# Kernel optimization log

Hardware: AMD Instinct MI355X
Metric: run time of the kernel (lower is better)

Reference implementation:

```python
import jax, jax.numpy as jnp
import numpy as np

CELL = 0.5          # grid_map cell size (meters)
NUM_POSES = 256     # config.num_pose_samples


def setup_inputs() -> dict:
    key = jax.random.key(0)
    k1, k2, k3, k4 = jax.random.split(key, 4)
    B, N, I, J, D = 2, 1024, 128, 128, 32
    f_q = jax.random.normal(k1, (B, N, D), jnp.float32)
    f_map = jax.random.normal(k2, (B, I, J, D), jnp.float32)
    # query frustum points: 32x32 grid, x in [-15.5, 15.5], y in [0.5, 31.5]
    xs = jnp.arange(32, dtype=jnp.float32) - 15.5
    ys = jnp.arange(32, dtype=jnp.float32) + 0.5
    grid = jnp.stack(jnp.meshgrid(xs, ys, indexing='ij'), -1).reshape(-1, 2)
    q_xy = jnp.broadcast_to(grid, (B, N, 2)).astype(jnp.float32)
    valid_q = jax.random.bernoulli(k3, 0.9, (B, N))
    valid_map = jax.random.bernoulli(k4, 0.8, (B, I, J))
    temperature = jnp.array(0.5, jnp.float32)
    return {"f_q": f_q, "f_map": f_map, "q_xy": q_xy, "temperature": temperature,
            "valid_q": valid_q, "valid_map": valid_map, "seed": 0}


def reference(f_q, f_map, q_xy, temperature, valid_q, valid_map, seed):
    B, N, D = f_q.shape
    _, I, J, _ = f_map.shape
    K = NUM_POSES

    # dense cross-correlation: [B, N, I, J]
    sim = jnp.einsum('bnd,bijd->bnij', f_q, f_map)
    sim = jax.nn.relu(sim)                      # clip_negative_scores
    sim = sim.astype(jnp.float32) * jnp.exp(temperature)
    # joint softmax over the two spatial axes
    m = sim.max(axis=(-2, -1), keepdims=True)
    e = jnp.exp(sim - m)
    prob = e / e.sum(axis=(-2, -1), keepdims=True)
    num_valid = valid_q.sum(-1).clip(min=1).astype(jnp.float32)[:, None, None, None]
    sim = sim / num_valid
    prob = prob / num_valid

    # --- RANSAC 2-point pose sampling (no gradient through prob) ---
    p = jax.lax.stop_gradient(prob)
    kq, km = jax.random.split(jax.random.key(seed))
    n_idx = jax.random.randint(kq, (B, 2 * K), 0, N)          # 2 query pts per pose
    b_idx = jnp.arange(B)[:, None]
    p_flat = p.reshape(B, N, I * J)
    rows = p_flat[b_idx, n_idx]                               # [B, 2K, IJ]
    m_flat = jax.random.categorical(km, jnp.log(rows + 1e-20), axis=-1)  # [B, 2K]
    mi, mj = m_flat // J, m_flat % J
    m_xy = (jnp.stack([mi, mj], -1).astype(jnp.float32) + 0.5) * CELL    # cell centers
    m_xy = m_xy.reshape(B, K, 2, 2)
    q_pts = q_xy[b_idx, n_idx].reshape(B, K, 2, 2)
    dq = q_pts[:, :, 1] - q_pts[:, :, 0]
    dm = m_xy[:, :, 1] - m_xy[:, :, 0]
    theta = jnp.arctan2(dm[..., 1], dm[..., 0]) - jnp.arctan2(dq[..., 1], dq[..., 0])
    c, s = jnp.cos(theta), jnp.sin(theta)
    R = jnp.stack([jnp.stack([c, -s], -1), jnp.stack([s, c], -1)], -2)   # [B,K,2,2]
    t = m_xy[:, :, 0] - jnp.einsum('bkxy,bky->bkx', R, q_pts[:, :, 0])   # [B,K,2]

    # --- score every pose hypothesis ---
    p_map = jnp.einsum('bkxy,bny->bknx', R, q_xy) + t[:, :, None]        # [B,K,N,2]
    ij = jnp.floor(p_map / CELL).astype(jnp.int32)
    inb = (ij[..., 0] >= 0) & (ij[..., 0] < I) & (ij[..., 1] >= 0) & (ij[..., 1] < J)
    flat = jnp.clip(ij[..., 0], 0, I - 1) * J + jnp.clip(ij[..., 1], 0, J - 1)  # [B,K,N]
    vmap_flat = valid_map.reshape(B, I * J)
    vgather = vmap_flat[b_idx, flat.reshape(B, K * N)].reshape(B, K, N)
    sim_flat = sim.reshape(B, N, I * J)
    sgather = jnp.take_along_axis(sim_flat, flat.transpose(0, 2, 1), axis=2)  # [B,N,K]
    mask = valid_q[:, None, :] & inb & vgather                                # [B,K,N]
    scores = jnp.sum(sgather.transpose(0, 2, 1) * mask, axis=-1)              # [B,K]
    return scores
```

## Files before the change

kernel.cpp:

```cpp
#include <hip/hip_runtime.h>
#include <stdint.h>

typedef unsigned int u32;
typedef unsigned long long u64;
typedef _Float16 f16x8 __attribute__((ext_vector_type(8)));
typedef float f32x4 __attribute__((ext_vector_type(4)));

#define IJ 16384
#define NQ 1024
#define NB 2
#define KP 256
#define NSEG 16
#define SEGW 1024
#define NT 1024

__device__ __forceinline__ void tf2x32(u32 k0, u32 k1, u32& x0, u32& x1) {
  u32 kx = k0 ^ k1 ^ 0x1BD11BDAu;
#define TFR(r) { x0 += x1; x1 = (x1 << (r)) | (x1 >> (32 - (r))); x1 ^= x0; }
  x0 += k0; x1 += k1;
  TFR(13) TFR(15) TFR(26) TFR(6)
  x0 += k1; x1 += kx + 1u;
  TFR(17) TFR(29) TFR(16) TFR(24)
  x0 += kx; x1 += k0 + 2u;
  TFR(13) TFR(15) TFR(26) TFR(6)
  x0 += k0; x1 += k1 + 3u;
  TFR(17) TFR(29) TFR(16) TFR(24)
  x0 += k1; x1 += kx + 4u;
  TFR(13) TFR(15) TFR(26) TFR(6)
  x0 += kx; x1 += k0 + 5u;
#undef TFR
}

__device__ __forceinline__ void tf_subkey(u32 k0, u32 k1, u32 i, u32& s0, u32& s1) {
  u32 x0 = 0u, x1 = i;
  tf2x32(k0, k1, x0, x1);
  s0 = x0; s1 = x1;
}

__device__ __forceinline__ u32 tf_xorbits(u32 k0, u32 k1, u32 i) {
  u32 x0 = 0u, x1 = i;
  tf2x32(k0, k1, x0, x1);
  return x0 ^ x1;
}

__device__ __forceinline__ void derive_keys(int seed, u32& kq0, u32& kq1,
                                            u32& km0, u32& km1) {
  u32 k0 = 0u;
  u32 k1 = (u32)seed;
  tf_subkey(k0, k1, 0u, kq0, kq1);
  tf_subkey(k0, k1, 1u, km0, km1);
}

__device__ __forceinline__ int derive_n(int seed, u32 s) {
  u32 kq0, kq1, km0, km1;
  derive_keys(seed, kq0, kq1, km0, km1);
  u32 l0, l1;
  tf_subkey(kq0, kq1, 1u, l0, l1);
  return (int)(tf_xorbits(l0, l1, s) & 1023u);
}

__device__ __forceinline__ float gumbel_from_bits(u32 w) {
  const float tiny = 1.17549435e-38f;
  float fl = __uint_as_float((w >> 9) | 0x3f800000u) - 1.0f;
  float u = fl * (1.0f - tiny) + tiny;
  u = fmaxf(tiny, u);
  return -logf(-logf(u));
}

__device__ __forceinline__ bool read_bool(const void* p, int idx, int is32) {
  return is32 ? (((const int*)p)[idx] != 0)
              : (((const unsigned char*)p)[idx] != 0);
}

__device__ __forceinline__ u32 fkey(float x) {
  u32 b = __float_as_uint(x);
  return b ^ ((b & 0x80000000u) ? 0xFFFFFFFFu : 0x80000000u);
}

__device__ __forceinline__ void load_split(const float* __restrict__ src,
                                           f16x8& h1, f16x8& h2) {
  float4 a = *(const float4*)src;
  float4 b = *(const float4*)(src + 16);
  float x[8] = {a.x, a.y, a.z, a.w, b.x, b.y, b.z, b.w};
#pragma unroll
  for (int e = 0; e < 8; ++e) {
    _Float16 hi = (_Float16)x[e];
    h1[e] = hi;
    h2[e] = (_Float16)((x[e] - (float)hi) * 2048.0f);
  }
}

__device__ __forceinline__ f32x4 emul_mfma(f16x8 m1, f16x8 m2, f16x8 q1,
                                           f16x8 q2) {
  const f32x4 zero4 = {0.f, 0.f, 0.f, 0.f};
  const float c11 = 4.8828125e-4f;
  f32x4 x = __builtin_amdgcn_mfma_f32_16x16x32_f16(m2, q2, zero4, 0, 0, 0);
  x *= c11;
  x = __builtin_amdgcn_mfma_f32_16x16x32_f16(m2, q1, x, 0, 0, 0);
  x = __builtin_amdgcn_mfma_f32_16x16x32_f16(m1, q2, x, 0, 0, 0);
  x *= c11;
  return __builtin_amdgcn_mfma_f32_16x16x32_f16(m1, q1, x, 0, 0, 0);
}

__global__ __launch_bounds__(256) void stats_kernel(
    const float* __restrict__ f_q, const float* __restrict__ f_map,
    const float* __restrict__ temp, const void* __restrict__ valid_q,
    const int* __restrict__ seedp, float* __restrict__ chunkmax,
    float* __restrict__ rowsum_part, u64* __restrict__ best,
    float* __restrict__ num_valid, int* __restrict__ bool_is32) {
  __shared__ int sred[256];
  __shared__ int is32_s;
  const int bx = blockIdx.x;
  const int by = blockIdx.y;
  const int tid = threadIdx.x;
  const int w = tid >> 6, l = tid & 63, l15 = l & 15, g = l >> 4;
  const int b = by >> 3;
  const int tp = by * 64 + w * 16 + l15;
  const int n = derive_n(seedp[0], (u32)tp);
  f16x8 q1, q2;
  load_split(f_q + ((size_t)b * NQ + n) * 32 + g * 4, q1, q2);
  const float et = expf(temp[0]);
  float rm = 0.f, se = 0.f;
#pragma unroll
  for (int T = 0; T < 16; ++T) {
    f16x8 m1, m2;
    load_split(f_map + ((size_t)b * IJ + (bx * 16 + T) * 16 + l15) * 32 + g * 4,
               m1, m2);
    f32x4 r = emul_mfma(m1, m2, q1, q2);
#pragma unroll
    for (int j = 0; j < 4; ++j) {
      float v = fmaxf(r[j], 0.f) * et;
      rm = fmaxf(rm, v);
      se += __expf(v);
    }
  }
  se += __shfl_xor(se, 16, 64);
  rm = fmaxf(rm, __shfl_xor(rm, 16, 64));
  se += __shfl_xor(se, 32, 64);
  rm = fmaxf(rm, __shfl_xor(rm, 32, 64));
  if (g == 0) {
    chunkmax[(size_t)tp * 64 + bx] = rm;
    rowsum_part[(size_t)tp * 64 + bx] = se;
  }
  if (bx == 0 && by == 0) {
    __syncthreads();
    for (int i = tid; i < NT; i += 256) best[i] = 0ull;
    const unsigned char* vb = (const unsigned char*)valid_q;
    int ones = 0;
    for (int i = tid; i < 2048; i += 256) ones += (vb[i] == 1) ? 1 : 0;
    sred[tid] = ones;
    __syncthreads();
    for (int off = 128; off > 0; off >>= 1) {
      if (tid < off) sred[tid] += sred[tid + off];
      __syncthreads();
    }
    if (tid == 0) {
      is32_s = (sred[0] < 1152) ? 1 : 0;
      bool_is32[0] = is32_s;
    }
    __syncthreads();
    const int is32 = is32_s;
    for (int bb = 0; bb < 2; ++bb) {
      int acc = 0;
      for (int i = tid; i < NQ; i += 256)
        acc += read_bool(valid_q, bb * NQ + i, is32) ? 1 : 0;
      sred[tid] = acc;
      __syncthreads();
      for (int off = 128; off > 0; off >>= 1) {
        if (tid < off) sred[tid] += sred[tid + off];
        __syncthreads();
      }
      if (tid == 0) {
        float nv = (float)sred[0];
        num_valid[bb] = nv < 1.f ? 1.f : nv;
      }
      __syncthreads();
    }
  }
}

__global__ __launch_bounds__(256) void select_kernel(
    const float* __restrict__ f_q, const float* __restrict__ f_map,
    const float* __restrict__ temp, const float* __restrict__ chunkmax,
    const float* __restrict__ rowsum_part, const float* __restrict__ num_valid,
    const int* __restrict__ seedp, u64* __restrict__ best) {
  __shared__ float mrow[16], srow[16];
  __shared__ u64 lbest[16];
  __shared__ int cnt;
  __shared__ u32 candk[4096];
  __shared__ float candv[4096];
  const int seg = blockIdx.x;
  const int tg = blockIdx.y;
  const int tid = threadIdx.x;
  const int w = tid >> 6, l = tid & 63, l15 = l & 15, g = l >> 4;
  const int b = tg >> 5;
  const int t0 = tg * 16;
  u32 kq0, kq1, km0, km1;
  derive_keys(seedp[0], kq0, kq1, km0, km1);
  if (tid < 16) {
    const float* cm = chunkmax + (size_t)(t0 + tid) * 64;
    const float* rp = rowsum_part + (size_t)(t0 + tid) * 64;
    float m = 0.f;
#pragma unroll
    for (int c = 0; c < 64; ++c) m = fmaxf(m, cm[c]);
    float s = 0.f;
#pragma unroll
    for (int c = 0; c < 64; ++c) s += rp[c];
    mrow[tid] = m;
    srow[tid] = s * expf(-m);
    lbest[tid] = 0ull;
  }
  if (tid == 0) cnt = 0;
  const int n = derive_n(seedp[0], (u32)(t0 + l15));
  f16x8 q1, q2;
  load_split(f_q + ((size_t)b * NQ + n) * 32 + g * 4, q1, q2);
  const float et = expf(temp[0]);
  const float nv = num_valid[b];
  __syncthreads();
  const float th = mrow[l15] - 22.0f;

  for (int sc = 0; sc < 4; ++sc) {
#pragma unroll
    for (int i = 0; i < 4; ++i) {
      const int Tl = sc * 16 + w * 4 + i;
      f16x8 m1, m2;
      load_split(
          f_map + ((size_t)b * IJ + seg * SEGW + Tl * 16 + l15) * 32 + g * 4,
          m1, m2);
      f32x4 r = emul_mfma(m1, m2, q1, q2);
#pragma unroll
      for (int j = 0; j < 4; ++j) {
        float v = fmaxf(r[j], 0.f) * et;
        if (v > th) {
          int p = atomicAdd(&cnt, 1);
          candk[p] = ((u32)l15 << 12) | (u32)(Tl * 16 + g * 4 + j);
          candv[p] = v;
        }
      }
    }
    __syncthreads();
    const int C = cnt;
    for (int c = tid; c < C; c += 256) {
      const u32 e = candk[c];
      const int r = (int)(e >> 12);
      const int f = seg * SEGW + (int)(e & 4095u);
      const float val = candv[c];
      const u32 wb = tf_xorbits(km0, km1, (u32)((t0 + r) * IJ + f));
      const float gmb = gumbel_from_bits(wb);
      const float v = logf((expf(val - mrow[r]) / srow[r]) / nv + 1e-20f) + gmb;
      const u64 key = ((u64)fkey(v) << 32) | (u64)(0xFFFFFFFFu - (u32)f);
      atomicMax(&lbest[r], key);
    }
    __syncthreads();
    if (tid == 0) cnt = 0;
    __syncthreads();
  }
  if (tid < 16) atomicMax(&best[t0 + tid], lbest[tid]);
}

__global__ __launch_bounds__(256) void score_kernel(
    const float* __restrict__ f_q, const float* __restrict__ f_map,
    const float* __restrict__ q_xy, const void* __restrict__ valid_q,
    const void* __restrict__ valid_map, const float* __restrict__ num_valid,
    const float* __restrict__ temp, const u64* __restrict__ best,
    const int* __restrict__ seedp, const int* __restrict__ bool_is32,
    float* __restrict__ out) {
  __shared__ float sred[256];
  __shared__ float4 Psh;
  const int idx = blockIdx.x;
  const int tid = threadIdx.x;
  const int b = idx >> 8, k = idx & 255;
  if (tid == 0) {
    const int t0 = b * 512 + 2 * k, t1 = t0 + 1;
    const int na = derive_n(seedp[0], (u32)t0);
    const int nb = derive_n(seedp[0], (u32)t1);
    const float2 q0 = ((const float2*)q_xy)[(size_t)b * NQ + na];
    const float2 q1 = ((const float2*)q_xy)[(size_t)b * NQ + nb];
    const int ma = (int)(0xFFFFFFFFu - (u32)(best[t0] & 0xFFFFFFFFu));
    const int mb = (int)(0xFFFFFFFFu - (u32)(best[t1] & 0xFFFFFFFFu));
    const float m0x = ((float)(ma >> 7) + 0.5f) * 0.5f;
    const float m0y = ((float)(ma & 127) + 0.5f) * 0.5f;
    const float m1x = ((float)(mb >> 7) + 0.5f) * 0.5f;
    const float m1y = ((float)(mb & 127) + 0.5f) * 0.5f;
    const float dqx = q1.x - q0.x, dqy = q1.y - q0.y;
    const float dmx = m1x - m0x, dmy = m1y - m0y;
    const float theta = atan2f(dmy, dmx) - atan2f(dqy, dqx);
    const float c = cosf(theta), s = sinf(theta);
    const float tx = m0x - (c * q0.x - s * q0.y);
    const float ty = m0y - (s * q0.x + c * q0.y);
    Psh = make_float4(c, s, tx, ty);
  }
  __syncthreads();
  const float4 P = Psh;
  const int is32 = bool_is32[0];
  const float et = expf(temp[0]);
  float acc = 0.f;
  for (int n = tid; n < NQ; n += 256) {
    float2 q = ((const float2*)q_xy)[(size_t)b * NQ + n];
    float px = P.x * q.x - P.y * q.y + P.z;
    float py = P.y * q.x + P.x * q.y + P.w;
    int ii = (int)floorf(px * 2.0f);
    int jj = (int)floorf(py * 2.0f);
    bool inb = (ii >= 0) & (ii < 128) & (jj >= 0) & (jj < 128);
    int ic = min(max(ii, 0), 127), jc = min(max(jj, 0), 127);
    int flat = (ic << 7) + jc;
    bool msk = read_bool(valid_q, b * NQ + n, is32) && inb &&
               read_bool(valid_map, b * IJ + flat, is32);
    if (msk) {
      const float4* A = (const float4*)(f_q + ((size_t)b * NQ + n) * 32);
      const float4* Bm = (const float4*)(f_map + ((size_t)b * IJ + flat) * 32);
      float4 s4 = {0.f, 0.f, 0.f, 0.f};
#pragma unroll
      for (int r = 0; r < 8; ++r) {
        float4 a = A[r], bb = Bm[r];
        s4.x = fmaf(a.x, bb.x, s4.x);
        s4.y = fmaf(a.y, bb.y, s4.y);
        s4.z = fmaf(a.z, bb.z, s4.z);
        s4.w = fmaf(a.w, bb.w, s4.w);
      }
      float dot = (s4.x + s4.y) + (s4.z + s4.w);
      acc += fmaxf(dot, 0.f) * et;
    }
  }
  sred[tid] = acc;
  __syncthreads();
  for (int off = 128; off > 0; off >>= 1) {
    if (tid < off) sred[tid] += sred[tid + off];
    __syncthreads();
  }
  if (tid == 0) out[idx] = sred[0] / num_valid[b];
}

extern "C" void kernel_launch(void* const* d_in, const int* in_sizes, int n_in,
                              void* d_out, int out_size, void* d_ws,
                              size_t ws_size, hipStream_t stream) {
  const float* f_q = (const float*)d_in[0];
  const float* f_map = (const float*)d_in[1];
  const float* q_xy = (const float*)d_in[2];
  const float* temp = (const float*)d_in[3];
  const void* valid_q = d_in[4];
  const void* valid_map = d_in[5];
  const int* seedp = (const int*)d_in[6];
  float* out = (float*)d_out;

  char* ws = (char*)d_ws;
  float* chunkmax = (float*)ws;
  float* rowsum_part = (float*)(ws + 262144);
  u64* best = (u64*)(ws + 524288);
  float* num_valid = (float*)(ws + 532480);
  int* bool_is32 = (int*)(ws + 532544);

  stats_kernel<<<dim3(64, 16), 256, 0, stream>>>(
      f_q, f_map, temp, valid_q, seedp, chunkmax, rowsum_part, best, num_valid,
      bool_is32);
  select_kernel<<<dim3(NSEG, 64), 256, 0, stream>>>(
      f_q, f_map, temp, chunkmax, rowsum_part, num_valid, seedp, best);
  score_kernel<<<NB * KP, 256, 0, stream>>>(f_q, f_map, q_xy, valid_q,
                                            valid_map, num_valid, temp, best,
                                            seedp, bool_is32, out);
}
```

Before: 138.0 us.

## Cache split fp16 map tiles in MFMA layout for select kernel; aggregate candidate atomics

The stats kernel now writes the hi/lo fp16 split of f_map, already arranged in the per-lane MFMA operand layout, to a workspace buffer. One row of blocks per batch does these writes. The select kernel then reads those pre-split vectors directly instead of reloading f32 f_map and converting it again. Candidate appends to shared memory now use a wavefront ballot so each wave issues one atomicAdd, and the atomicMax on lbest is skipped when the key cannot win. The cost is an extra 4MB of workspace writes in the stats kernel, and the select kernel now depends on that data being written first.

```diff
diff --git a/kernel.cpp b/kernel.cpp
--- a/kernel.cpp
+++ b/kernel.cpp
@@ -107,7 +107,8 @@
     const float* __restrict__ temp, const void* __restrict__ valid_q,
     const int* __restrict__ seedp, float* __restrict__ chunkmax,
     float* __restrict__ rowsum_part, u64* __restrict__ best,
-    float* __restrict__ num_valid, int* __restrict__ bool_is32) {
+    float* __restrict__ num_valid, int* __restrict__ bool_is32,
+    _Float16* __restrict__ ms1, _Float16* __restrict__ ms2) {
   __shared__ int sred[256];
   __shared__ int is32_s;
   const int bx = blockIdx.x;
@@ -120,12 +121,18 @@
   f16x8 q1, q2;
   load_split(f_q + ((size_t)b * NQ + n) * 32 + g * 4, q1, q2);
   const float et = expf(temp[0]);
+  const bool writer = ((by & 7) == 0);
   float rm = 0.f, se = 0.f;
 #pragma unroll
   for (int T = 0; T < 16; ++T) {
     f16x8 m1, m2;
     load_split(f_map + ((size_t)b * IJ + (bx * 16 + T) * 16 + l15) * 32 + g * 4,
                m1, m2);
+    if (writer) {
+      const size_t toff = ((size_t)(b * 1024 + bx * 16 + T) * 64 + l) * 8;
+      *(f16x8*)(ms1 + toff) = m1;
+      *(f16x8*)(ms2 + toff) = m2;
+    }
     f32x4 r = emul_mfma(m1, m2, q1, q2);
 #pragma unroll
     for (int j = 0; j < 4; ++j) {
@@ -180,10 +187,11 @@
 }
 
 __global__ __launch_bounds__(256) void select_kernel(
-    const float* __restrict__ f_q, const float* __restrict__ f_map,
-    const float* __restrict__ temp, const float* __restrict__ chunkmax,
-    const float* __restrict__ rowsum_part, const float* __restrict__ num_valid,
-    const int* __restrict__ seedp, u64* __restrict__ best) {
+    const _Float16* __restrict__ ms1, const _Float16* __restrict__ ms2,
+    const float* __restrict__ f_q, const float* __restrict__ temp,
+    const float* __restrict__ chunkmax, const float* __restrict__ rowsum_part,
+    const float* __restrict__ num_valid, const int* __restrict__ seedp,
+    u64* __restrict__ best) {
   __shared__ float mrow[16], srow[16];
   __shared__ u64 lbest[16];
   __shared__ int cnt;
@@ -223,18 +231,26 @@
 #pragma unroll
     for (int i = 0; i < 4; ++i) {
       const int Tl = sc * 16 + w * 4 + i;
-      f16x8 m1, m2;
-      load_split(
-          f_map + ((size_t)b * IJ + seg * SEGW + Tl * 16 + l15) * 32 + g * 4,
-          m1, m2);
+      const size_t moff = ((size_t)(b * 1024 + seg * 64 + Tl) * 64 + l) * 8;
+      const f16x8 m1 = *(const f16x8*)(ms1 + moff);
+      const f16x8 m2 = *(const f16x8*)(ms2 + moff);
       f32x4 r = emul_mfma(m1, m2, q1, q2);
 #pragma unroll
       for (int j = 0; j < 4; ++j) {
-        float v = fmaxf(r[j], 0.f) * et;
-        if (v > th) {
-          int p = atomicAdd(&cnt, 1);
-          candk[p] = ((u32)l15 << 12) | (u32)(Tl * 16 + g * 4 + j);
-          candv[p] = v;
+        const float v = fmaxf(r[j], 0.f) * et;
+        const bool pred = v > th;
+        const u64 mask = __ballot(pred);
+        if (mask) {
+          const int leader = (int)(__ffsll((unsigned long long)mask) - 1);
+          int wbase = 0;
+          if (l == leader) wbase = atomicAdd(&cnt, (int)__popcll(mask));
+          wbase = __shfl(wbase, leader, 64);
+          if (pred) {
+            const int pos =
+                wbase + (int)__popcll(mask & ((1ull << l) - 1ull));
+            candk[pos] = ((u32)l15 << 12) | (u32)(Tl * 16 + g * 4 + j);
+            candv[pos] = v;
+          }
         }
       }
     }
@@ -249,7 +265,7 @@
       const float gmb = gumbel_from_bits(wb);
       const float v = logf((expf(val - mrow[r]) / srow[r]) / nv + 1e-20f) + gmb;
       const u64 key = ((u64)fkey(v) << 32) | (u64)(0xFFFFFFFFu - (u32)f);
-      atomicMax(&lbest[r], key);
+      if (key > lbest[r]) atomicMax(&lbest[r], key);
     }
     __syncthreads();
     if (tid == 0) cnt = 0;
@@ -344,17 +360,19 @@
   float* out = (float*)d_out;
 
   char* ws = (char*)d_ws;
-  float* chunkmax = (float*)ws;
-  float* rowsum_part = (float*)(ws + 262144);
-  u64* best = (u64*)(ws + 524288);
-  float* num_valid = (float*)(ws + 532480);
-  int* bool_is32 = (int*)(ws + 532544);
+  _Float16* ms1 = (_Float16*)ws;
+  _Float16* ms2 = (_Float16*)(ws + 2097152);
+  float* chunkmax = (float*)(ws + 4194304);
+  float* rowsum_part = (float*)(ws + 4456448);
+  u64* best = (u64*)(ws + 4718592);
+  float* num_valid = (float*)(ws + 4726784);
+  int* bool_is32 = (int*)(ws + 4726848);
 
   stats_kernel<<<dim3(64, 16), 256, 0, stream>>>(
       f_q, f_map, temp, valid_q, seedp, chunkmax, rowsum_part, best, num_valid,
-      bool_is32);
+      bool_is32, ms1, ms2);
   select_kernel<<<dim3(NSEG, 64), 256, 0, stream>>>(
-      f_q, f_map, temp, chunkmax, rowsum_part, num_valid, seedp, best);
+      ms1, ms2, f_q, temp, chunkmax, rowsum_part, num_valid, seedp, best);
   score_kernel<<<NB * KP, 256, 0, stream>>>(f_q, f_map, q_xy, valid_q,
                                             valid_map, num_valid, temp, best,
                                             seedp, bool_is32, out);
```

Result: slower. 145.1 us (+5.2%).
